# Kernel tuning notes

Hardware: AMD Instinct MI355X
Metric: run time of the kernel (lower is better)

## Reference

```python
import jax, jax.numpy as jnp
import numpy as np

DIM = 1024
NUM_HEADS = 16
BATCH = 4
SEQ = 2048
SCALE = (DIM // NUM_HEADS) ** -0.5
MASK_VAL = -10000000.0


def setup_inputs() -> dict:
    key = jax.random.key(0)
    k1, k2, k3, k4 = jax.random.split(key, 4)
    inputs = jax.random.normal(k1, (BATCH, SEQ, DIM), dtype=jnp.float32)
    # xavier-ish scaling for weights
    W_qkv = jax.random.normal(k2, (3 * DIM, DIM), dtype=jnp.float32) * (1.0 / np.sqrt(DIM))
    W_fc = jax.random.normal(k3, (DIM, DIM), dtype=jnp.float32) * (1.0 / np.sqrt(DIM))
    b_fc = jnp.zeros((DIM,), dtype=jnp.float32)
    padding_mask = jax.random.randint(k4, (BATCH, SEQ), 0, 2, dtype=jnp.int32)
    return {"inputs": inputs, "W_qkv": W_qkv, "W_fc": W_fc, "b_fc": b_fc,
            "padding_mask": padding_mask}


def reference(inputs, W_qkv, W_fc, b_fc, padding_mask):
    B, N, C = inputs.shape
    H = NUM_HEADS
    Dh = C // H
    # qkv projection (torch Linear: x @ W.T), [B,N,3C]
    qkv = jnp.einsum('bnc,oc->bno', inputs, W_qkv)
    qkv = qkv.reshape(B, N, 3, H, Dh).transpose(2, 0, 3, 1, 4)  # [3,B,H,N,Dh]
    q, k, v = qkv[0], qkv[1], qkv[2]
    att = jnp.einsum('bhqd,bhkd->bhqk', q, k) * SCALE  # [B,H,N,N]
    mask = padding_mask[:, None, None, :]              # [B,1,1,N]
    att = jnp.where(mask > 0, jnp.float32(MASK_VAL), att)
    att = jax.nn.softmax(att, axis=-1)
    x = jnp.einsum('bhqk,bhkd->bhqd', att, v)          # [B,H,N,Dh]
    x = x.transpose(0, 2, 1, 3).reshape(B, N, C)       # [B,N,C]
    out = jnp.einsum('bnc,oc->bno', x, W_fc) + b_fc
    return out
```

## Files before the change

kernel.cpp:

```cpp
#include <hip/hip_runtime.h>
#include <stdint.h>

constexpr int kDim  = 1024;
constexpr int kH    = 16;
constexpr int kB    = 4;
constexpr int kSeq  = 2048;
constexpr int kDh   = 64;
constexpr int kMTot = kB * kSeq;
constexpr int kNQkv = 3 * kDim;
constexpr float kScale = 0.125f;
constexpr float kLog2e = 1.44269504088896f;
constexpr float kC1    = kScale * kLog2e;
constexpr float kMaxSub = 10.0f;
constexpr float kMk2Un   = -kMaxSub * kLog2e;
constexpr float kMk2Mask = -1.0e9f;
constexpr int kPld = 72;
constexpr int kCld = 136;

typedef __attribute__((ext_vector_type(8))) short short8;
typedef __attribute__((ext_vector_type(4))) float floatx4;

__device__ __forceinline__ unsigned short f2bf(float f) {
  union { float f; unsigned u; } v; v.f = f;
  unsigned r = v.u + 0x7fffu + ((v.u >> 16) & 1u);
  return (unsigned short)(r >> 16);
}
__device__ __forceinline__ unsigned short f2bf_fast(float f) {
  union { float f; unsigned u; } v; v.f = f;
  return (unsigned short)((v.u + 0x8000u) >> 16);
}
__device__ __forceinline__ float vexp2(float x) {
  float r; asm("v_exp_f32 %0, %1" : "=v"(r) : "v"(x)); return r;
}
__device__ __forceinline__ void gl2lds16(const void* g, void* l) {
  __builtin_amdgcn_global_load_lds(
      (const __attribute__((address_space(1))) unsigned int*)g,
      (__attribute__((address_space(3))) unsigned int*)l, 16, 0, 0);
}

__global__ void __launch_bounds__(256) cvt_scan(
    const float4* __restrict__ x, const float4* __restrict__ wq,
    const float4* __restrict__ wf,
    ushort4* __restrict__ xb, ushort4* __restrict__ wqb, ushort4* __restrict__ wfb,
    const int* __restrict__ pm, int* __restrict__ cidx, int* __restrict__ nkd) {
  const int X4  = (kMTot * kDim) / 4;
  const int WQ4 = (kNQkv * kDim) / 4;
  const int NCVT = 12288;
  if (blockIdx.x >= NCVT) {
    const int b = blockIdx.x - NCVT;
    const int t = threadIdx.x;
    const int lane = t & 63, wv = t >> 6;
    __shared__ int wsum[4];
    __shared__ int woff[5];
    int base = t * 8;
    int keep[8]; int cnt = 0;
#pragma unroll
    for (int j = 0; j < 8; j++) {
      keep[j] = (pm[b * kSeq + base + j] <= 0) ? 1 : 0;
      cnt += keep[j];
    }
    int pre = cnt;
#pragma unroll
    for (int off = 1; off < 64; off <<= 1) {
      int v = __shfl_up(pre, off, 64);
      if (lane >= off) pre += v;
    }
    int excl = pre - cnt;
    if (lane == 63) wsum[wv] = pre;
    __syncthreads();
    if (t == 0) {
      int s = 0;
#pragma unroll
      for (int w = 0; w < 4; w++) { woff[w] = s; s += wsum[w]; }
      woff[4] = s;
      nkd[b] = s;
    }
    __syncthreads();
    const int nk = woff[4];
    int kp = woff[wv] + excl;
#pragma unroll
    for (int j = 0; j < 8; j++) {
      int n = base + j;
      int pos = keep[j] ? kp : nk + (n - kp);
      cidx[b * kSeq + pos] = b * kSeq + n;
      kp += keep[j];
    }
    return;
  }
  int i = blockIdx.x * 256 + threadIdx.x;
  float4 v; ushort4* dst;
  if (i < X4)            { v = x[i];             dst = xb  + i; }
  else if (i < X4 + WQ4) { v = wq[i - X4];       dst = wqb + (i - X4); }
  else                   { v = wf[i - X4 - WQ4]; dst = wfb + (i - X4 - WQ4); }
  ushort4 o;
  o.x = f2bf(v.x); o.y = f2bf(v.y); o.z = f2bf(v.z); o.w = f2bf(v.w);
  *dst = o;
}

__device__ __forceinline__ void gemm128_mainloop(
    const unsigned short* const arow[4], const unsigned short* __restrict__ Bw,
    int tN, unsigned short* As, unsigned short* Bs, floatx4 acc[4][4]) {
  const int t = threadIdx.x;
  const int lane = t & 63, wv = t >> 6;
  const int wm = (wv >> 1) << 6, wn = (wv & 1) << 6;
  const int lrow = lane & 15, quad = lane >> 4, l7 = lane & 7;
  const int srow = t >> 3;
  const int pu8 = (t & 7) * 8;
  const int lu8 = ((t & 7) ^ (srow & 7)) * 8;
  const int off0 = (quad ^ l7) * 8;

  floatx4 zero = {0.f, 0.f, 0.f, 0.f};
#pragma unroll
  for (int mi = 0; mi < 4; mi++)
#pragma unroll
    for (int ni = 0; ni < 4; ni++) acc[mi][ni] = zero;

  for (int k0 = 0; k0 < kDim; k0 += 64) {
#pragma unroll
    for (int p = 0; p < 4; ++p) {
      int r = srow + p * 32;
      gl2lds16(arow[p] + k0 + lu8, As + r * 64 + pu8);
      gl2lds16(Bw + (int64_t)(tN + r) * kDim + k0 + lu8, Bs + r * 64 + pu8);
    }
    __syncthreads();
#pragma unroll
    for (int kk = 0; kk < 64; kk += 32) {
      short8 af[4], bf[4];
#pragma unroll
      for (int mi = 0; mi < 4; mi++)
        af[mi] = *(const short8*)(As + (wm + mi * 16 + lrow) * 64 + (off0 ^ kk));
#pragma unroll
      for (int ni = 0; ni < 4; ni++)
        bf[ni] = *(const short8*)(Bs + (wn + ni * 16 + lrow) * 64 + (off0 ^ kk));
#pragma unroll
      for (int mi = 0; mi < 4; mi++)
#pragma unroll
        for (int ni = 0; ni < 4; ni++)
          acc[mi][ni] = __builtin_amdgcn_mfma_f32_16x16x32_bf16(af[mi], bf[ni], acc[mi][ni], 0, 0, 0);
    }
    __syncthreads();
  }
}

__global__ void __launch_bounds__(256) gemm_qkv(
    const unsigned short* __restrict__ xb, const unsigned short* __restrict__ wqb,
    const int* __restrict__ cidx, const int* __restrict__ nkd,
    unsigned short* __restrict__ qb, unsigned short* __restrict__ kb,
    unsigned short* __restrict__ vtb) {
  const int tN = blockIdx.x * 128, tM = blockIdx.y * 128;
  const int which = tN >> 10;
  if (which != 0) {
    int b = tM >> 11, local = tM & 2047;
    if (local >= nkd[b]) return;
  }
  extern __shared__ __attribute__((aligned(16))) unsigned short smem[];
  unsigned short* As = smem;
  unsigned short* Bs = smem + 128 * 64;
  floatx4 acc[4][4];

  const int t = threadIdx.x, srow = t >> 3;
  const unsigned short* arow[4];
#pragma unroll
  for (int p = 0; p < 4; p++) {
    int r = tM + srow + p * 32;
    int rid = (which == 0) ? r : cidx[r];
    arow[p] = xb + (int64_t)rid * kDim;
  }
  gemm128_mainloop(arow, wqb, tN, As, Bs, acc);

  const int lane = t & 63, wv = t >> 6;
  const int wm = (wv >> 1) << 6, wn = (wv & 1) << 6;
  const int lrow = lane & 15, quad = lane >> 4;
  unsigned short* Cs = smem;
  const bool vblk = (which == 2);
#pragma unroll
  for (int ni = 0; ni < 4; ni++) {
    int c = wn + ni * 16 + lrow;
#pragma unroll
    for (int mi = 0; mi < 4; mi++) {
#pragma unroll
      for (int r = 0; r < 4; r++) {
        int row = wm + mi * 16 + quad * 4 + r;
        unsigned short val = f2bf(acc[mi][ni][r]);
        if (!vblk) Cs[row * kCld + c] = val;
        else       Cs[c * kCld + row] = val;
      }
    }
  }
  __syncthreads();
  const int mj8 = lane >> 3;
  const int chunk = lane & 7;
#pragma unroll
  for (int half = 0; half < 2; half++) {
#pragma unroll
    for (int g = 0; g < 4; g++) {
      int mjr = wv * 32 + g * 8 + mj8;
      short8 vec = *(const short8*)(Cs + mjr * kCld + half * 64 + chunk * 8);
      if (!vblk) {
        int i = tM + mjr;
        int bb = i >> 11, n = i & 2047;
        int o = tN + half * 64 + chunk * 8;
        int h = (o >> 6) & 15;
        int64_t base = (int64_t)((bb << 4) + h) << 17;
        unsigned short* dst = (which == 0 ? qb : kb) + base + (int64_t)n * 64 + (o & 63);
        *(short8*)dst = vec;
      } else {
        int o = tN + mjr;
        int h = (o >> 6) & 15, d = o & 63;
        int bb = tM >> 11;
        int n0 = (tM & 2047) + half * 64 + chunk * 8;
        unsigned short* dst = vtb + (((int64_t)((bb << 4) + h)) << 17)
                              + (int64_t)d * 2048 + n0;
        *(short8*)dst = vec;
      }
    }
  }
}

__global__ void __launch_bounds__(256, 4) attn(
    const unsigned short* __restrict__ qb, const unsigned short* __restrict__ kb,
    const unsigned short* __restrict__ vtb, const int* __restrict__ nkd,
    unsigned short* __restrict__ xab) {
  __shared__ __attribute__((aligned(16))) unsigned short Ks[64 * 64];
  __shared__ __attribute__((aligned(16))) unsigned short Vs[64 * 64];
  __shared__ __attribute__((aligned(16))) unsigned short Ps[4][2][16 * kPld];

  const int t = threadIdx.x, lane = t & 63, wv = t >> 6;
  const int lrow = lane & 15, quad = lane >> 4, l7 = lane & 7;
  const int qblk = blockIdx.x & 15, bh = blockIdx.x >> 4;
  const int b = bh >> 4, h = bh & 15;
  const int q0 = qblk * 128;
  const int srow = t >> 3;
  const int pu8 = (t & 7) * 8;
  const int lu8 = ((t & 7) ^ (srow & 7)) * 8;
  const int off0 = (quad ^ l7) * 8;

  const int nk  = nkd[b];
  const int nkt = (nk + 63) >> 6;

  const unsigned short* Qb0 = qb + ((int64_t)bh * kSeq + q0 + wv * 16 + lrow) * kDh;
  short8 qf[2][2];
  qf[0][0] = *(const short8*)(Qb0 + quad * 8);
  qf[0][1] = *(const short8*)(Qb0 + 32 + quad * 8);
  qf[1][0] = *(const short8*)(Qb0 + 64 * kDh + quad * 8);
  qf[1][1] = *(const short8*)(Qb0 + 64 * kDh + 32 + quad * 8);

  float l_run[2][4];
  floatx4 o_acc[2][4];
  floatx4 zero = {0.f, 0.f, 0.f, 0.f};
#pragma unroll
  for (int t2 = 0; t2 < 2; t2++) {
#pragma unroll
    for (int r = 0; r < 4; r++) l_run[t2][r] = 0.f;
#pragma unroll
    for (int di = 0; di < 4; di++) o_acc[t2][di] = zero;
  }

  const unsigned short* Kbase = kb  + (int64_t)bh * kSeq * kDh;
  const unsigned short* Vbase = vtb + (int64_t)bh * kDh * kSeq;

  for (int kt = 0; kt < nkt; ++kt) {
    const int k0 = kt * 64;
    {
      int r0 = srow, r1 = srow + 32;
      gl2lds16(Kbase + (int64_t)(k0 + r0) * kDh + lu8, Ks + r0 * 64 + pu8);
      gl2lds16(Kbase + (int64_t)(k0 + r1) * kDh + lu8, Ks + r1 * 64 + pu8);
      gl2lds16(Vbase + (int64_t)r0 * kSeq + k0 + lu8,  Vs + r0 * 64 + pu8);
      gl2lds16(Vbase + (int64_t)r1 * kSeq + k0 + lu8,  Vs + r1 * 64 + pu8);
    }
    __syncthreads();

    floatx4 s[2][4];
#pragma unroll
    for (int ni = 0; ni < 4; ni++) {
      const unsigned short* Kr = Ks + (ni * 16 + lrow) * 64;
      short8 kf0 = *(const short8*)(Kr + off0);
      short8 kf1 = *(const short8*)(Kr + (off0 ^ 32));
#pragma unroll
      for (int t2 = 0; t2 < 2; t2++) {
        floatx4 tmp = __builtin_amdgcn_mfma_f32_16x16x32_bf16(qf[t2][0], kf0, zero, 0, 0, 0);
        s[t2][ni]   = __builtin_amdgcn_mfma_f32_16x16x32_bf16(qf[t2][1], kf1, tmp, 0, 0, 0);
      }
    }
    float mk2[4];
#pragma unroll
    for (int c = 0; c < 4; c++)
      mk2[c] = (k0 + c * 16 + lrow < nk) ? kMk2Un : kMk2Mask;

#pragma unroll
    for (int t2 = 0; t2 < 2; t2++) {
      unsigned short* Pw = &Ps[wv][t2][0];
#pragma unroll
      for (int r = 0; r < 4; r++) {
        int prow = (quad * 4 + r) * kPld + lrow;
#pragma unroll
        for (int c = 0; c < 4; c++) {
          float p = vexp2(fmaf(s[t2][c][r], kC1, mk2[c]));
          l_run[t2][r] += p;
          Pw[prow + c * 16] = f2bf_fast(p);
        }
      }
    }
    asm volatile("s_waitcnt lgkmcnt(0)" ::: "memory");

#pragma unroll
    for (int ks = 0; ks < 2; ks++) {
      short8 pf0 = *(const short8*)(&Ps[wv][0][0] + lrow * kPld + ks * 32 + quad * 8);
      short8 pf1 = *(const short8*)(&Ps[wv][1][0] + lrow * kPld + ks * 32 + quad * 8);
      const int voff = off0 ^ (ks * 32);
#pragma unroll
      for (int di = 0; di < 4; di++) {
        short8 vf = *(const short8*)(Vs + (di * 16 + lrow) * 64 + voff);
        o_acc[0][di] = __builtin_amdgcn_mfma_f32_16x16x32_bf16(pf0, vf, o_acc[0][di], 0, 0, 0);
        o_acc[1][di] = __builtin_amdgcn_mfma_f32_16x16x32_bf16(pf1, vf, o_acc[1][di], 0, 0, 0);
      }
    }
    __syncthreads();
  }

#pragma unroll
  for (int t2 = 0; t2 < 2; t2++) {
#pragma unroll
    for (int r = 0; r < 4; r++) {
      float l = l_run[t2][r];
      l += __shfl_xor(l, 1, 64);
      l += __shfl_xor(l, 2, 64);
      l += __shfl_xor(l, 4, 64);
      l += __shfl_xor(l, 8, 64);
      float inv = 1.0f / l;
      int n = q0 + t2 * 64 + wv * 16 + quad * 4 + r;
      int64_t rowbase = ((int64_t)b * kSeq + n) * kDim + h * kDh;
#pragma unroll
      for (int di = 0; di < 4; di++)
        xab[rowbase + di * 16 + lrow] = f2bf(o_acc[t2][di][r] * inv);
    }
  }
}

__global__ void __launch_bounds__(256) gemm_fc(
    const unsigned short* __restrict__ xab, const unsigned short* __restrict__ wfb,
    const float* __restrict__ bfc, float* __restrict__ out) {
  __shared__ __attribute__((aligned(16))) unsigned short As[128 * 64];
  __shared__ __attribute__((aligned(16))) unsigned short Bs[128 * 64];
  floatx4 acc[4][4];
  const int tN = blockIdx.x * 128, tM = blockIdx.y * 128;
  const int t = threadIdx.x, srow = t >> 3;
  const unsigned short* arow[4];
#pragma unroll
  for (int p = 0; p < 4; p++)
    arow[p] = xab + (int64_t)(tM + srow + p * 32) * kDim;
  gemm128_mainloop(arow, wfb, tN, As, Bs, acc);

  const int lane = t & 63, wv = t >> 6;
  const int wm = (wv >> 1) << 6, wn = (wv & 1) << 6;
  const int lrow = lane & 15, quad = lane >> 4;
#pragma unroll
  for (int ni = 0; ni < 4; ni++) {
    int o = tN + wn + ni * 16 + lrow;
    float bias = bfc[o];
#pragma unroll
    for (int mi = 0; mi < 4; mi++) {
#pragma unroll
      for (int r = 0; r < 4; r++) {
        int i = tM + wm + mi * 16 + quad * 4 + r;
        out[(int64_t)i * kDim + o] = acc[mi][ni][r] + bias;
      }
    }
  }
}

extern "C" void kernel_launch(void* const* d_in, const int* in_sizes, int n_in,
                              void* d_out, int out_size, void* d_ws, size_t ws_size,
                              hipStream_t stream) {
  (void)in_sizes; (void)n_in; (void)out_size; (void)ws_size;
  const float* x    = (const float*)d_in[0];
  const float* wqkv = (const float*)d_in[1];
  const float* wfc  = (const float*)d_in[2];
  const float* bfc  = (const float*)d_in[3];
  const int*   pm   = (const int*)d_in[4];
  float* out = (float*)d_out;

  char* ws = (char*)d_ws;
  unsigned short* xb  = (unsigned short*)(ws);
  unsigned short* wqb = (unsigned short*)(ws + 16777216);
  unsigned short* wfb = (unsigned short*)(ws + 23068672);
  unsigned short* qb  = (unsigned short*)(ws + 25165824);
  unsigned short* kb  = (unsigned short*)(ws + 41943040);
  unsigned short* vtb = (unsigned short*)(ws + 58720256);
  int*            cidx= (int*)(ws + 75497472);
  int*            nkd = (int*)(ws + 75530240);
  unsigned short* xab = xb;

  cvt_scan<<<12288 + kB, 256, 0, stream>>>(
      (const float4*)x, (const float4*)wqkv, (const float4*)wfc,
      (ushort4*)xb, (ushort4*)wqb, (ushort4*)wfb, pm, cidx, nkd);
  gemm_qkv<<<dim3(kNQkv / 128, kMTot / 128), 256, 128 * kCld * 2, stream>>>(
      xb, wqb, cidx, nkd, qb, kb, vtb);
  attn<<<kB * kH * (kSeq / 128), 256, 0, stream>>>(qb, kb, vtb, nkd, xab);
  gemm_fc<<<dim3(kDim / 128, kMTot / 128), 256, 0, stream>>>(xab, wfb, bfc, out);
}
```

Measured before the change: 242.8 us.

## Shrink QKV epilogue smem via two-pass staging and use 128x64 tiles for FC GEMM

The QKV GEMM epilogue now stages the output tile through shared memory in two 64-row/column halves. This cuts dynamic shared memory from about 34KB to 32KB, and the launch bounds now request 5 blocks per CU to raise occupancy. It costs one extra barrier. The FC GEMM switches to 128x64 output tiles with its own inlined main loop, which doubles the grid to improve CU fill and shrinks the B shared tile, at the cost of less reuse of each A tile.

```diff
diff --git a/kernel.cpp b/kernel.cpp
--- a/kernel.cpp
+++ b/kernel.cpp
@@ -142,7 +142,7 @@
   }
 }
 
-__global__ void __launch_bounds__(256) gemm_qkv(
+__global__ void __launch_bounds__(256, 5) gemm_qkv(
     const unsigned short* __restrict__ xb, const unsigned short* __restrict__ wqb,
     const int* __restrict__ cidx, const int* __restrict__ nkd,
     unsigned short* __restrict__ qb, unsigned short* __restrict__ kb,
@@ -173,45 +173,51 @@
   const int lrow = lane & 15, quad = lane >> 4;
   unsigned short* Cs = smem;
   const bool vblk = (which == 2);
-#pragma unroll
-  for (int ni = 0; ni < 4; ni++) {
-    int c = wn + ni * 16 + lrow;
-#pragma unroll
-    for (int mi = 0; mi < 4; mi++) {
-#pragma unroll
-      for (int r = 0; r < 4; r++) {
-        int row = wm + mi * 16 + quad * 4 + r;
-        unsigned short val = f2bf(acc[mi][ni][r]);
-        if (!vblk) Cs[row * kCld + c] = val;
-        else       Cs[c * kCld + row] = val;
-      }
-    }
-  }
-  __syncthreads();
-  const int mj8 = lane >> 3;
-  const int chunk = lane & 7;
-#pragma unroll
-  for (int half = 0; half < 2; half++) {
-#pragma unroll
-    for (int g = 0; g < 4; g++) {
-      int mjr = wv * 32 + g * 8 + mj8;
-      short8 vec = *(const short8*)(Cs + mjr * kCld + half * 64 + chunk * 8);
-      if (!vblk) {
-        int i = tM + mjr;
-        int bb = i >> 11, n = i & 2047;
-        int o = tN + half * 64 + chunk * 8;
-        int h = (o >> 6) & 15;
-        int64_t base = (int64_t)((bb << 4) + h) << 17;
-        unsigned short* dst = (which == 0 ? qb : kb) + base + (int64_t)n * 64 + (o & 63);
-        *(short8*)dst = vec;
-      } else {
-        int o = tN + mjr;
-        int h = (o >> 6) & 15, d = o & 63;
-        int bb = tM >> 11;
-        int n0 = (tM & 2047) + half * 64 + chunk * 8;
-        unsigned short* dst = vtb + (((int64_t)((bb << 4) + h)) << 17)
-                              + (int64_t)d * 2048 + n0;
-        *(short8*)dst = vec;
+  const int mj8 = lane >> 3, chunk = lane & 7;
+#pragma unroll
+  for (int pass = 0; pass < 2; pass++) {
+    if (pass) __syncthreads();
+    bool mine = vblk ? ((wv & 1) == pass) : ((wv >> 1) == pass);
+    if (mine) {
+#pragma unroll
+      for (int ni = 0; ni < 4; ni++) {
+        int c = wn + ni * 16 + lrow;
+#pragma unroll
+        for (int mi = 0; mi < 4; mi++) {
+#pragma unroll
+          for (int r = 0; r < 4; r++) {
+            int row = wm + mi * 16 + quad * 4 + r;
+            unsigned short val = f2bf(acc[mi][ni][r]);
+            if (!vblk) Cs[(row - pass * 64) * kCld + c] = val;
+            else       Cs[(c - pass * 64) * kCld + row] = val;
+          }
+        }
+      }
+    }
+    __syncthreads();
+#pragma unroll
+    for (int half = 0; half < 2; half++) {
+#pragma unroll
+      for (int g = 0; g < 2; g++) {
+        int ml = wv * 16 + g * 8 + mj8;
+        short8 vec = *(const short8*)(Cs + ml * kCld + half * 64 + chunk * 8);
+        if (!vblk) {
+          int i = tM + pass * 64 + ml;
+          int bb = i >> 11, n = i & 2047;
+          int o = tN + half * 64 + chunk * 8;
+          int h = (o >> 6) & 15;
+          int64_t base = (int64_t)((bb << 4) + h) << 17;
+          unsigned short* dst = (which == 0 ? qb : kb) + base + (int64_t)n * 64 + (o & 63);
+          *(short8*)dst = vec;
+        } else {
+          int o = tN + pass * 64 + ml;
+          int h = (o >> 6) & 15, d = o & 63;
+          int bb = tM >> 11;
+          int n0 = (tM & 2047) + half * 64 + chunk * 8;
+          unsigned short* dst = vtb + (((int64_t)((bb << 4) + h)) << 17)
+                                + (int64_t)d * 2048 + n0;
+          *(short8*)dst = vec;
+        }
       }
     }
   }
@@ -341,21 +347,56 @@
     const unsigned short* __restrict__ xab, const unsigned short* __restrict__ wfb,
     const float* __restrict__ bfc, float* __restrict__ out) {
   __shared__ __attribute__((aligned(16))) unsigned short As[128 * 64];
-  __shared__ __attribute__((aligned(16))) unsigned short Bs[128 * 64];
-  floatx4 acc[4][4];
-  const int tN = blockIdx.x * 128, tM = blockIdx.y * 128;
-  const int t = threadIdx.x, srow = t >> 3;
-  const unsigned short* arow[4];
-#pragma unroll
-  for (int p = 0; p < 4; p++)
-    arow[p] = xab + (int64_t)(tM + srow + p * 32) * kDim;
-  gemm128_mainloop(arow, wfb, tN, As, Bs, acc);
-
+  __shared__ __attribute__((aligned(16))) unsigned short Bs[64 * 64];
+  const int tN = blockIdx.x * 64, tM = blockIdx.y * 128;
+  const int t = threadIdx.x;
   const int lane = t & 63, wv = t >> 6;
-  const int wm = (wv >> 1) << 6, wn = (wv & 1) << 6;
-  const int lrow = lane & 15, quad = lane >> 4;
-#pragma unroll
-  for (int ni = 0; ni < 4; ni++) {
+  const int wm = (wv >> 1) << 6, wn = (wv & 1) << 5;
+  const int lrow = lane & 15, quad = lane >> 4, l7 = lane & 7;
+  const int srow = t >> 3;
+  const int pu8 = (t & 7) * 8;
+  const int lu8 = ((t & 7) ^ (srow & 7)) * 8;
+  const int off0 = (quad ^ l7) * 8;
+
+  floatx4 acc[4][2];
+  floatx4 zero = {0.f, 0.f, 0.f, 0.f};
+#pragma unroll
+  for (int mi = 0; mi < 4; mi++)
+#pragma unroll
+    for (int ni = 0; ni < 2; ni++) acc[mi][ni] = zero;
+
+  for (int k0 = 0; k0 < kDim; k0 += 64) {
+#pragma unroll
+    for (int p = 0; p < 4; ++p) {
+      int r = srow + p * 32;
+      gl2lds16(xab + (int64_t)(tM + r) * kDim + k0 + lu8, As + r * 64 + pu8);
+    }
+#pragma unroll
+    for (int p = 0; p < 2; ++p) {
+      int r = srow + p * 32;
+      gl2lds16(wfb + (int64_t)(tN + r) * kDim + k0 + lu8, Bs + r * 64 + pu8);
+    }
+    __syncthreads();
+#pragma unroll
+    for (int kk = 0; kk < 64; kk += 32) {
+      short8 af[4], bf[2];
+#pragma unroll
+      for (int mi = 0; mi < 4; mi++)
+        af[mi] = *(const short8*)(As + (wm + mi * 16 + lrow) * 64 + (off0 ^ kk));
+#pragma unroll
+      for (int ni = 0; ni < 2; ni++)
+        bf[ni] = *(const short8*)(Bs + (wn + ni * 16 + lrow) * 64 + (off0 ^ kk));
+#pragma unroll
+      for (int mi = 0; mi < 4; mi++)
+#pragma unroll
+        for (int ni = 0; ni < 2; ni++)
+          acc[mi][ni] = __builtin_amdgcn_mfma_f32_16x16x32_bf16(af[mi], bf[ni], acc[mi][ni], 0, 0, 0);
+    }
+    __syncthreads();
+  }
+
+#pragma unroll
+  for (int ni = 0; ni < 2; ni++) {
     int o = tN + wn + ni * 16 + lrow;
     float bias = bfc[o];
 #pragma unroll
@@ -394,8 +435,8 @@
   cvt_scan<<<12288 + kB, 256, 0, stream>>>(
       (const float4*)x, (const float4*)wqkv, (const float4*)wfc,
       (ushort4*)xb, (ushort4*)wqb, (ushort4*)wfb, pm, cidx, nkd);
-  gemm_qkv<<<dim3(kNQkv / 128, kMTot / 128), 256, 128 * kCld * 2, stream>>>(
+  gemm_qkv<<<dim3(kNQkv / 128, kMTot / 128), 256, 32768, stream>>>(
       xb, wqb, cidx, nkd, qb, kb, vtb);
   attn<<<kB * kH * (kSeq / 128), 256, 0, stream>>>(qb, kb, vtb, nkd, xab);
-  gemm_fc<<<dim3(kDim / 128, kMTot / 128), 256, 0, stream>>>(xab, wfb, bfc, out);
-}
+  gemm_fc<<<dim3(kDim / 64, kMTot / 128), 256, 0, stream>>>(xab, wfb, bfc, out);
+}
```

Result: slower. 347.9 us (+43.3%).
